# Kernel tuning notes

Hardware: AMD Instinct MI355X
Metric: run time of the kernel (lower is better)

## Reference

```python
import jax, jax.numpy as jnp
import numpy as np

B, SQ, SK, D, H = 4, 2048, 2048, 1024, 16
HD = D // H


def setup_inputs() -> dict:
    key = jax.random.key(0)
    ks = jax.random.split(key, 12)
    s = 1.0 / np.sqrt(D)
    return {
        "query": jax.random.normal(ks[0], (B, SQ, D), jnp.float32),
        "key": jax.random.normal(ks[1], (B, SK, D), jnp.float32),
        "value": jax.random.normal(ks[2], (B, SK, D), jnp.float32),
        "key_padding_mask": jax.random.randint(ks[3], (B, SK), 0, 2, jnp.int32),
        "Wq": jax.random.uniform(ks[4], (D, D), jnp.float32, -s, s),
        "bq": jnp.zeros((D,), jnp.float32),
        "Wk": jax.random.uniform(ks[5], (D, D), jnp.float32, -s, s),
        "bk": jnp.zeros((D,), jnp.float32),
        "Wv": jax.random.uniform(ks[6], (D, D), jnp.float32, -s, s),
        "bv": jnp.zeros((D,), jnp.float32),
        "Wo": jax.random.uniform(ks[7], (D, D), jnp.float32, -s, s),
        "bo": jnp.zeros((D,), jnp.float32),
    }


def reference(query, key, value, key_padding_mask, Wq, bq, Wk, bk, Wv, bv, Wo, bo):
    scale = HD ** -0.5
    # projections: torch Linear is x @ W.T + b
    q = (query @ Wq.T + bq).reshape(B, SQ, H, HD).transpose(0, 2, 1, 3)  # [B,H,SQ,HD]
    k = (key @ Wk.T + bk).reshape(B, SK, H, HD).transpose(0, 2, 1, 3)    # [B,H,SK,HD]
    v = (value @ Wv.T + bv).reshape(B, SK, H, HD).transpose(0, 2, 1, 3)  # [B,H,SK,HD]
    scores = jnp.einsum("bhqd,bhkd->bhqk", q, k) * scale                  # [B,H,SQ,SK]
    mask = key_padding_mask[:, None, None, :] != 0                        # True = keep
    scores = jnp.where(mask, scores, -jnp.inf)
    attn = jax.nn.softmax(scores, axis=-1)
    # dropout is identity at inference (eval mode)
    out = jnp.einsum("bhqk,bhkd->bhqd", attn, v)                          # [B,H,SQ,HD]
    out = out.transpose(0, 2, 1, 3).reshape(B, SQ, D)
    return out @ Wo.T + bo
```

## Files before the change

kernel.cpp:

```cpp
#include <hip/hip_runtime.h>


typedef __bf16 bf16_t;
typedef __attribute__((ext_vector_type(4))) __bf16 bf16x4;
typedef __attribute__((ext_vector_type(8))) __bf16 bf16x8;
typedef __attribute__((ext_vector_type(4))) float f32x4;

#define MFMA16(a, b, c) __builtin_amdgcn_mfma_f32_16x16x32_bf16(a, b, c, 0, 0, 0)

__device__ __forceinline__ void gl_lds16(const void* g, void* l) {
  __builtin_amdgcn_global_load_lds(
      (const __attribute__((address_space(1))) unsigned int*)g,
      (__attribute__((address_space(3))) unsigned int*)l, 16, 0, 0);
}

__global__ void wconv_kernel(const float* __restrict__ Wq, const float* __restrict__ Wk,
                             const float* __restrict__ Wv, const float* __restrict__ Wo,
                             bf16_t* __restrict__ out) {
  const int m = blockIdx.y;
  const float* src = (m == 0) ? Wq : (m == 1) ? Wk : (m == 2) ? Wv : Wo;
  bf16_t* dst = out + (size_t)m * (1024 * 1024);
  const int idx = (blockIdx.x * 256 + threadIdx.x) * 4;
  float4 v = *(const float4*)(src + idx);
  bf16x4 pk;
  pk[0] = (bf16_t)v.x; pk[1] = (bf16_t)v.y; pk[2] = (bf16_t)v.z; pk[3] = (bf16_t)v.w;
  *(bf16x4*)(dst + idx) = pk;
}

template <bool A_F32>
__global__ __launch_bounds__(256, 2) void gemm_kernel(
    const void* __restrict__ Aptr, const bf16_t* __restrict__ Bw,
    const float* __restrict__ bias, void* __restrict__ outp, const int out_mode) {
  __shared__ __align__(16) bf16_t As[2][16 * 512];
  __shared__ __align__(16) bf16_t Bs[2][16 * 512];

  const int tid = threadIdx.x;
  const int lane = tid & 63, wave = tid >> 6;
  const int fm = lane & 15, quad = lane >> 4;
  const int wr = wave >> 1, wc = wave & 1;
  const int m0 = blockIdx.x * 128, n0 = blockIdx.y * 128;

  f32x4 acc[4][4];
#pragma unroll
  for (int i = 0; i < 4; ++i)
#pragma unroll
    for (int j = 0; j < 4; ++j) acc[i][j] = f32x4{0.f, 0.f, 0.f, 0.f};

  auto stage = [&](int ks, int buf) {
    const int k0 = ks * 64;
    if constexpr (A_F32) {
      const float* A = (const float*)Aptr;
#pragma unroll
      for (int it = 0; it < 4; ++it) {
        const int fid = wave * 4 + it;
        const int row = (fid >> 1) * 16 + fm;
        const int col = (fid & 1) * 32 + quad * 8;
        const float* src = A + (size_t)(m0 + row) * 1024 + k0 + col;
        float4 v0 = *(const float4*)src, v1 = *(const float4*)(src + 4);
        bf16x8 pk;
        pk[0] = (bf16_t)v0.x; pk[1] = (bf16_t)v0.y; pk[2] = (bf16_t)v0.z; pk[3] = (bf16_t)v0.w;
        pk[4] = (bf16_t)v1.x; pk[5] = (bf16_t)v1.y; pk[6] = (bf16_t)v1.z; pk[7] = (bf16_t)v1.w;
        *(bf16x8*)(As[buf] + fid * 512 + lane * 8) = pk;
      }
    } else {
      const bf16_t* A = (const bf16_t*)Aptr;
#pragma unroll
      for (int it = 0; it < 4; ++it) {
        const int fid = wave * 4 + it;
        const int row = (fid >> 1) * 16 + fm;
        const int col = (fid & 1) * 32 + quad * 8;
        gl_lds16(A + (size_t)(m0 + row) * 1024 + k0 + col, As[buf] + fid * 512);
      }
    }
#pragma unroll
    for (int it = 0; it < 4; ++it) {
      const int fid = wave * 4 + it;
      const int row = (fid >> 1) * 16 + fm;
      const int col = (fid & 1) * 32 + quad * 8;
      gl_lds16(Bw + (size_t)(n0 + row) * 1024 + k0 + col, Bs[buf] + fid * 512);
    }
  };

  stage(0, 0);
  for (int ks = 0; ks < 16; ++ks) {
    __syncthreads();
    if (ks + 1 < 16) stage(ks + 1, (ks + 1) & 1);
    const bf16_t* Ab = As[ks & 1];
    const bf16_t* Bb = Bs[ks & 1];
#pragma unroll
    for (int u = 0; u < 2; ++u) {
      bf16x8 af[4], bfr[4];
#pragma unroll
      for (int i = 0; i < 4; ++i)
        af[i] = *(const bf16x8*)(Ab + ((4 * wr + i) * 2 + u) * 512 + lane * 8);
#pragma unroll
      for (int j = 0; j < 4; ++j)
        bfr[j] = *(const bf16x8*)(Bb + ((4 * wc + j) * 2 + u) * 512 + lane * 8);
#pragma unroll
      for (int i = 0; i < 4; ++i)
#pragma unroll
        for (int j = 0; j < 4; ++j) acc[i][j] = MFMA16(af[i], bfr[j], acc[i][j]);
    }
  }

  float bval[4];
#pragma unroll
  for (int j = 0; j < 4; ++j) bval[j] = bias[n0 + wc * 64 + j * 16 + fm];

#pragma unroll
  for (int i = 0; i < 4; ++i) {
#pragma unroll
    for (int j = 0; j < 4; ++j) {
      const int col = n0 + wc * 64 + j * 16 + fm;
#pragma unroll
      for (int r = 0; r < 4; ++r) {
        const int row = m0 + wr * 64 + i * 16 + quad * 4 + r;
        const float v = acc[i][j][r] + bval[j];
        if (out_mode == 2) {
          ((float*)outp)[(size_t)row * 1024 + col] = v;
        } else if (out_mode == 0) {
          ((bf16_t*)outp)[(size_t)row * 1024 + col] = (bf16_t)v;
        } else {
          const int bb = row >> 11, sk = row & 2047;
          const int tt = sk >> 7, L128 = sk & 127;
          const int c = L128 >> 5, hf = (L128 >> 4) & 1;
          const int qd = (L128 >> 2) & 3, rr = L128 & 3;
          const int hh = col >> 6, hd = col & 63;
          const int nt = hd >> 4, fv = hd & 15;
          const size_t idx = (((size_t)(bb * 16 + hh)) << 17) + tt * 8192 +
                             (nt * 4 + c) * 512 + (qd * 16 + fv) * 8 + hf * 4 + rr;
          ((bf16_t*)outp)[idx] = (bf16_t)v;
        }
      }
    }
  }
}

__global__ __launch_bounds__(256, 2) void attn_kernel(
    const bf16_t* __restrict__ q16, const bf16_t* __restrict__ k16,
    const bf16_t* __restrict__ vt16, const int* __restrict__ mask,
    bf16_t* __restrict__ o16) {
  __shared__ __align__(16) bf16_t Kb[2][8192];
  __shared__ __align__(16) bf16_t Vb[2][8192];
  __shared__ float mbuf[2][128];
  __shared__ float lbuf[128];

  const int tid = threadIdx.x;
  const int lane = tid & 63, wave = tid >> 6;
  const int fm = lane & 15, quad = lane >> 4;
  const int qt = blockIdx.x, bh = blockIdx.y;
  const int b = bh >> 4, h = bh & 15;
  const float SC = 0.125f * 1.44269504f;

  bf16x8 aq[2][2];
#pragma unroll
  for (int i = 0; i < 2; ++i)
#pragma unroll
    for (int dc = 0; dc < 2; ++dc) {
      const int row = qt * 128 + (2 * wave + i) * 16 + fm;
      aq[i][dc] = *(const bf16x8*)(q16 + ((size_t)(b * 2048 + row)) * 1024 + h * 64 +
                                   dc * 32 + quad * 8);
    }

  auto stageKV = [&](int t, int buf) {
    const bf16_t* kb = k16 + ((size_t)(b * 2048 + t * 128)) * 1024 + h * 64;
#pragma unroll
    for (int s = 0; s < 4; ++s) {
      const int fid = wave * 4 + s;
      const int row = (fid >> 1) * 16 + fm;
      const int col = (fid & 1) * 32 + quad * 8;
      gl_lds16(kb + (size_t)row * 1024 + col, Kb[buf] + fid * 512);
    }
    const bf16_t* vbase = vt16 + ((size_t)bh << 17) + t * 8192;
#pragma unroll
    for (int s = 0; s < 4; ++s) {
      const int fid = wave * 4 + s;
      gl_lds16(vbase + fid * 512 + lane * 8, Vb[buf] + fid * 512);
    }
    if (tid < 128) mbuf[buf][tid] = mask[b * 2048 + t * 128 + tid] ? 0.0f : -1e30f;
  };

  f32x4 oacc[2][4];
#pragma unroll
  for (int i = 0; i < 2; ++i)
#pragma unroll
    for (int n = 0; n < 4; ++n) oacc[i][n] = f32x4{0.f, 0.f, 0.f, 0.f};
  float lrow[2] = {0.f, 0.f};

  stageKV(0, 0);
  for (int t = 0; t < 16; ++t) {
    __syncthreads();
    if (t + 1 < 16) stageKV(t + 1, (t + 1) & 1);
    const bf16_t* K = Kb[t & 1];
    const bf16_t* V = Vb[t & 1];
    const float* mb = mbuf[t & 1];

    f32x4 sacc[2][8];
#pragma unroll
    for (int i = 0; i < 2; ++i)
#pragma unroll
      for (int j = 0; j < 8; ++j) sacc[i][j] = f32x4{0.f, 0.f, 0.f, 0.f};
#pragma unroll
    for (int j = 0; j < 8; ++j) {
#pragma unroll
      for (int dc = 0; dc < 2; ++dc) {
        bf16x8 kf = *(const bf16x8*)(K + (j * 2 + dc) * 512 + lane * 8);
        sacc[0][j] = MFMA16(kf, aq[0][dc], sacc[0][j]);
        sacc[1][j] = MFMA16(kf, aq[1][dc], sacc[1][j]);
      }
    }

#pragma unroll
    for (int j = 0; j < 8; ++j) {
      f32x4 md = *(const f32x4*)&mb[j * 16 + quad * 4];
#pragma unroll
      for (int i = 0; i < 2; ++i) {
#pragma unroll
        for (int r = 0; r < 4; ++r) {
          const float p = __builtin_amdgcn_exp2f(fmaf(sacc[i][j][r], SC, md[r]));
          sacc[i][j][r] = p;
          lrow[i] += p;
        }
      }
    }

#pragma unroll
    for (int c = 0; c < 4; ++c) {
      bf16x8 pf[2];
#pragma unroll
      for (int i = 0; i < 2; ++i) {
#pragma unroll
        for (int r = 0; r < 4; ++r) {
          pf[i][r] = (bf16_t)sacc[i][2 * c][r];
          pf[i][4 + r] = (bf16_t)sacc[i][2 * c + 1][r];
        }
      }
#pragma unroll
      for (int n = 0; n < 4; ++n) {
        bf16x8 vv = *(const bf16x8*)(V + (n * 4 + c) * 512 + lane * 8);
        oacc[0][n] = MFMA16(pf[0], vv, oacc[0][n]);
        oacc[1][n] = MFMA16(pf[1], vv, oacc[1][n]);
      }
    }
  }

#pragma unroll
  for (int i = 0; i < 2; ++i) {
    float l = lrow[i];
    l += __shfl_xor(l, 16);
    l += __shfl_xor(l, 32);
    if (quad == 0) lbuf[wave * 32 + i * 16 + fm] = l;
  }
  __syncthreads();
#pragma unroll
  for (int i = 0; i < 2; ++i) {
    f32x4 lv = *(const f32x4*)&lbuf[wave * 32 + i * 16 + quad * 4];
#pragma unroll
    for (int r = 0; r < 4; ++r) {
      const float inv = 1.0f / lv[r];
      const int row = qt * 128 + wave * 32 + i * 16 + quad * 4 + r;
#pragma unroll
      for (int n = 0; n < 4; ++n) {
        o16[((size_t)(b * 2048 + row)) * 1024 + h * 64 + n * 16 + fm] =
            (bf16_t)(oacc[i][n][r] * inv);
      }
    }
  }
}

extern "C" void kernel_launch(void* const* d_in, const int* in_sizes, int n_in,
                              void* d_out, int out_size, void* d_ws, size_t ws_size,
                              hipStream_t stream) {
  const float* query = (const float*)d_in[0];
  const float* key   = (const float*)d_in[1];
  const float* value = (const float*)d_in[2];
  const int* mask    = (const int*)d_in[3];
  const float* Wq = (const float*)d_in[4];
  const float* bq = (const float*)d_in[5];
  const float* Wk = (const float*)d_in[6];
  const float* bk = (const float*)d_in[7];
  const float* Wv = (const float*)d_in[8];
  const float* bv = (const float*)d_in[9];
  const float* Wo = (const float*)d_in[10];
  const float* bo = (const float*)d_in[11];

  char* ws = (char*)d_ws;
  bf16_t* W16  = (bf16_t*)ws;
  bf16_t* q16  = (bf16_t*)(ws + (size_t)8 * 1024 * 1024);
  bf16_t* k16  = q16 + 8388608;
  bf16_t* vt16 = k16 + 8388608;
  bf16_t* o16  = vt16 + 8388608;

  wconv_kernel<<<dim3(1024, 4), 256, 0, stream>>>(Wq, Wk, Wv, Wo, W16);
  gemm_kernel<true><<<dim3(64, 8), 256, 0, stream>>>(query, W16,           bq, q16,  0);
  gemm_kernel<true><<<dim3(64, 8), 256, 0, stream>>>(key,   W16 + 1048576, bk, k16,  0);
  gemm_kernel<true><<<dim3(64, 8), 256, 0, stream>>>(value, W16 + 2097152, bv, vt16, 1);
  attn_kernel<<<dim3(16, 64), 256, 0, stream>>>(q16, k16, vt16, mask, o16);
  gemm_kernel<false><<<dim3(64, 8), 256, 0, stream>>>(o16, W16 + 3145728, bo, d_out, 2);
}
```

Before: 420.3 us.

## Merge QKV projections, pipeline A loads via registers, restructure attention staging

Merges the three input projection GEMMs into a single launch with a z-dimension. The fp32 A tile is now loaded into registers before the MFMA loop and converted and written to LDS after it, so its global latency overlaps compute; packed bf16 conversion is used. In attention, V becomes single-buffered with an extra barrier to cut LDS and target three blocks per CU, the mask is loaded vectorized, and row sums come from an MFMA against ones instead of a shuffle reduction. The extra per-tile barrier and a single V buffer may expose more load latency.

```diff
diff --git a/kernel.cpp b/kernel.cpp
--- a/kernel.cpp
+++ b/kernel.cpp
@@ -2,6 +2,7 @@
 
 
 typedef __bf16 bf16_t;
+typedef __attribute__((ext_vector_type(2))) __bf16 bf16x2;
 typedef __attribute__((ext_vector_type(4))) __bf16 bf16x4;
 typedef __attribute__((ext_vector_type(8))) __bf16 bf16x8;
 typedef __attribute__((ext_vector_type(4))) float f32x4;
@@ -12,6 +13,17 @@
   __builtin_amdgcn_global_load_lds(
       (const __attribute__((address_space(1))) unsigned int*)g,
       (__attribute__((address_space(3))) unsigned int*)l, 16, 0, 0);
+}
+
+__device__ __forceinline__ bf16x2 cvt_pk_bf16(float a, float b) {
+#if __has_builtin(__builtin_amdgcn_cvt_pk_bf16_f32)
+  return __builtin_amdgcn_cvt_pk_bf16_f32(a, b);
+#else
+  bf16x2 r;
+  r[0] = (bf16_t)a;
+  r[1] = (bf16_t)b;
+  return r;
+#endif
 }
 
 __global__ void wconv_kernel(const float* __restrict__ Wq, const float* __restrict__ Wk,
@@ -27,12 +39,18 @@
   *(bf16x4*)(dst + idx) = pk;
 }
 
-template <bool A_F32>
-__global__ __launch_bounds__(256, 2) void gemm_kernel(
-    const void* __restrict__ Aptr, const bf16_t* __restrict__ Bw,
-    const float* __restrict__ bias, void* __restrict__ outp, const int out_mode) {
-  __shared__ __align__(16) bf16_t As[2][16 * 512];
-  __shared__ __align__(16) bf16_t Bs[2][16 * 512];
+__global__ __launch_bounds__(256, 2) void proj_kernel(
+    const float* __restrict__ Aq, const float* __restrict__ Ak, const float* __restrict__ Av,
+    const bf16_t* __restrict__ W16,
+    const float* __restrict__ bq, const float* __restrict__ bk, const float* __restrict__ bv,
+    bf16_t* __restrict__ q16, bf16_t* __restrict__ k16, bf16_t* __restrict__ vt16) {
+  __shared__ __align__(16) bf16_t As[2][8192];
+  __shared__ __align__(16) bf16_t Bs[2][8192];
+
+  const int z = blockIdx.z;
+  const float* A = (z == 0) ? Aq : (z == 1) ? Ak : Av;
+  const bf16_t* Bw = W16 + (size_t)z * 1048576;
+  const float* bias = (z == 0) ? bq : (z == 1) ? bk : bv;
 
   const int tid = threadIdx.x;
   const int lane = tid & 63, wave = tid >> 6;
@@ -46,45 +64,51 @@
 #pragma unroll
     for (int j = 0; j < 4; ++j) acc[i][j] = f32x4{0.f, 0.f, 0.f, 0.f};
 
-  auto stage = [&](int ks, int buf) {
-    const int k0 = ks * 64;
-    if constexpr (A_F32) {
-      const float* A = (const float*)Aptr;
-#pragma unroll
-      for (int it = 0; it < 4; ++it) {
-        const int fid = wave * 4 + it;
-        const int row = (fid >> 1) * 16 + fm;
-        const int col = (fid & 1) * 32 + quad * 8;
-        const float* src = A + (size_t)(m0 + row) * 1024 + k0 + col;
-        float4 v0 = *(const float4*)src, v1 = *(const float4*)(src + 4);
-        bf16x8 pk;
-        pk[0] = (bf16_t)v0.x; pk[1] = (bf16_t)v0.y; pk[2] = (bf16_t)v0.z; pk[3] = (bf16_t)v0.w;
-        pk[4] = (bf16_t)v1.x; pk[5] = (bf16_t)v1.y; pk[6] = (bf16_t)v1.z; pk[7] = (bf16_t)v1.w;
-        *(bf16x8*)(As[buf] + fid * 512 + lane * 8) = pk;
-      }
-    } else {
-      const bf16_t* A = (const bf16_t*)Aptr;
-#pragma unroll
-      for (int it = 0; it < 4; ++it) {
-        const int fid = wave * 4 + it;
-        const int row = (fid >> 1) * 16 + fm;
-        const int col = (fid & 1) * 32 + quad * 8;
-        gl_lds16(A + (size_t)(m0 + row) * 1024 + k0 + col, As[buf] + fid * 512);
-      }
-    }
+  float4 areg[4][2];
+  auto loadA = [&](int ks) {
 #pragma unroll
     for (int it = 0; it < 4; ++it) {
       const int fid = wave * 4 + it;
       const int row = (fid >> 1) * 16 + fm;
       const int col = (fid & 1) * 32 + quad * 8;
-      gl_lds16(Bw + (size_t)(n0 + row) * 1024 + k0 + col, Bs[buf] + fid * 512);
-    }
-  };
-
-  stage(0, 0);
+      const float* s = A + (size_t)(m0 + row) * 1024 + ks * 64 + col;
+      areg[it][0] = *(const float4*)s;
+      areg[it][1] = *(const float4*)(s + 4);
+    }
+  };
+  auto writeA = [&](int buf) {
+#pragma unroll
+    for (int it = 0; it < 4; ++it) {
+      const int fid = wave * 4 + it;
+      bf16x8 pk;
+      bf16x2* p2 = (bf16x2*)&pk;
+      p2[0] = cvt_pk_bf16(areg[it][0].x, areg[it][0].y);
+      p2[1] = cvt_pk_bf16(areg[it][0].z, areg[it][0].w);
+      p2[2] = cvt_pk_bf16(areg[it][1].x, areg[it][1].y);
+      p2[3] = cvt_pk_bf16(areg[it][1].z, areg[it][1].w);
+      *(bf16x8*)(As[buf] + fid * 512 + lane * 8) = pk;
+    }
+  };
+  auto dmaB = [&](int ks, int buf) {
+#pragma unroll
+    for (int it = 0; it < 4; ++it) {
+      const int fid = wave * 4 + it;
+      const int row = (fid >> 1) * 16 + fm;
+      const int col = (fid & 1) * 32 + quad * 8;
+      gl_lds16(Bw + (size_t)(n0 + row) * 1024 + ks * 64 + col, Bs[buf] + fid * 512);
+    }
+  };
+
+  loadA(0);
+  writeA(0);
+  dmaB(0, 0);
+
   for (int ks = 0; ks < 16; ++ks) {
     __syncthreads();
-    if (ks + 1 < 16) stage(ks + 1, (ks + 1) & 1);
+    if (ks < 15) {
+      loadA(ks + 1);
+      dmaB(ks + 1, (ks + 1) & 1);
+    }
     const bf16_t* Ab = As[ks & 1];
     const bf16_t* Bb = Bs[ks & 1];
 #pragma unroll
@@ -101,12 +125,14 @@
 #pragma unroll
         for (int j = 0; j < 4; ++j) acc[i][j] = MFMA16(af[i], bfr[j], acc[i][j]);
     }
+    if (ks < 15) writeA((ks + 1) & 1);
   }
 
   float bval[4];
 #pragma unroll
   for (int j = 0; j < 4; ++j) bval[j] = bias[n0 + wc * 64 + j * 16 + fm];
 
+  bf16_t* outp = (z == 0) ? q16 : (z == 1) ? k16 : vt16;
 #pragma unroll
   for (int i = 0; i < 4; ++i) {
 #pragma unroll
@@ -116,10 +142,8 @@
       for (int r = 0; r < 4; ++r) {
         const int row = m0 + wr * 64 + i * 16 + quad * 4 + r;
         const float v = acc[i][j][r] + bval[j];
-        if (out_mode == 2) {
-          ((float*)outp)[(size_t)row * 1024 + col] = v;
-        } else if (out_mode == 0) {
-          ((bf16_t*)outp)[(size_t)row * 1024 + col] = (bf16_t)v;
+        if (z != 2) {
+          outp[(size_t)row * 1024 + col] = (bf16_t)v;
         } else {
           const int bb = row >> 11, sk = row & 2047;
           const int tt = sk >> 7, L128 = sk & 127;
@@ -129,21 +153,87 @@
           const int nt = hd >> 4, fv = hd & 15;
           const size_t idx = (((size_t)(bb * 16 + hh)) << 17) + tt * 8192 +
                              (nt * 4 + c) * 512 + (qd * 16 + fv) * 8 + hf * 4 + rr;
-          ((bf16_t*)outp)[idx] = (bf16_t)v;
+          outp[idx] = (bf16_t)v;
         }
       }
     }
   }
 }
 
-__global__ __launch_bounds__(256, 2) void attn_kernel(
+__global__ __launch_bounds__(256, 2) void oproj_kernel(
+    const bf16_t* __restrict__ A, const bf16_t* __restrict__ Bw,
+    const float* __restrict__ bias, float* __restrict__ outp) {
+  __shared__ __align__(16) bf16_t As[2][8192];
+  __shared__ __align__(16) bf16_t Bs[2][8192];
+
+  const int tid = threadIdx.x;
+  const int lane = tid & 63, wave = tid >> 6;
+  const int fm = lane & 15, quad = lane >> 4;
+  const int wr = wave >> 1, wc = wave & 1;
+  const int m0 = blockIdx.x * 128, n0 = blockIdx.y * 128;
+
+  f32x4 acc[4][4];
+#pragma unroll
+  for (int i = 0; i < 4; ++i)
+#pragma unroll
+    for (int j = 0; j < 4; ++j) acc[i][j] = f32x4{0.f, 0.f, 0.f, 0.f};
+
+  auto stage = [&](int ks, int buf) {
+#pragma unroll
+    for (int it = 0; it < 4; ++it) {
+      const int fid = wave * 4 + it;
+      const int row = (fid >> 1) * 16 + fm;
+      const int col = (fid & 1) * 32 + quad * 8;
+      gl_lds16(A + (size_t)(m0 + row) * 1024 + ks * 64 + col, As[buf] + fid * 512);
+      gl_lds16(Bw + (size_t)(n0 + row) * 1024 + ks * 64 + col, Bs[buf] + fid * 512);
+    }
+  };
+
+  stage(0, 0);
+  for (int ks = 0; ks < 16; ++ks) {
+    __syncthreads();
+    if (ks < 15) stage(ks + 1, (ks + 1) & 1);
+    const bf16_t* Ab = As[ks & 1];
+    const bf16_t* Bb = Bs[ks & 1];
+#pragma unroll
+    for (int u = 0; u < 2; ++u) {
+      bf16x8 af[4], bfr[4];
+#pragma unroll
+      for (int i = 0; i < 4; ++i)
+        af[i] = *(const bf16x8*)(Ab + ((4 * wr + i) * 2 + u) * 512 + lane * 8);
+#pragma unroll
+      for (int j = 0; j < 4; ++j)
+        bfr[j] = *(const bf16x8*)(Bb + ((4 * wc + j) * 2 + u) * 512 + lane * 8);
+#pragma unroll
+      for (int i = 0; i < 4; ++i)
+#pragma unroll
+        for (int j = 0; j < 4; ++j) acc[i][j] = MFMA16(af[i], bfr[j], acc[i][j]);
+    }
+  }
+
+  float bval[4];
+#pragma unroll
+  for (int j = 0; j < 4; ++j) bval[j] = bias[n0 + wc * 64 + j * 16 + fm];
+#pragma unroll
+  for (int i = 0; i < 4; ++i)
+#pragma unroll
+    for (int j = 0; j < 4; ++j) {
+      const int col = n0 + wc * 64 + j * 16 + fm;
+#pragma unroll
+      for (int r = 0; r < 4; ++r) {
+        const int row = m0 + wr * 64 + i * 16 + quad * 4 + r;
+        outp[(size_t)row * 1024 + col] = acc[i][j][r] + bval[j];
+      }
+    }
+}
+
+__global__ __launch_bounds__(256, 3) void attn_kernel(
     const bf16_t* __restrict__ q16, const bf16_t* __restrict__ k16,
     const bf16_t* __restrict__ vt16, const int* __restrict__ mask,
     bf16_t* __restrict__ o16) {
   __shared__ __align__(16) bf16_t Kb[2][8192];
-  __shared__ __align__(16) bf16_t Vb[2][8192];
-  __shared__ float mbuf[2][128];
-  __shared__ float lbuf[128];
+  __shared__ __align__(16) bf16_t Vb[8192];
+  __shared__ float mb[2][128];
 
   const int tid = threadIdx.x;
   const int lane = tid & 63, wave = tid >> 6;
@@ -162,7 +252,7 @@
                                    dc * 32 + quad * 8);
     }
 
-  auto stageKV = [&](int t, int buf) {
+  auto dmaK = [&](int t, int buf) {
     const bf16_t* kb = k16 + ((size_t)(b * 2048 + t * 128)) * 1024 + h * 64;
 #pragma unroll
     for (int s = 0; s < 4; ++s) {
@@ -171,13 +261,22 @@
       const int col = (fid & 1) * 32 + quad * 8;
       gl_lds16(kb + (size_t)row * 1024 + col, Kb[buf] + fid * 512);
     }
-    const bf16_t* vbase = vt16 + ((size_t)bh << 17) + t * 8192;
+  };
+  auto dmaV = [&](int t) {
+    const bf16_t* vb = vt16 + ((size_t)bh << 17) + t * 8192;
 #pragma unroll
     for (int s = 0; s < 4; ++s) {
       const int fid = wave * 4 + s;
-      gl_lds16(vbase + fid * 512 + lane * 8, Vb[buf] + fid * 512);
-    }
-    if (tid < 128) mbuf[buf][tid] = mask[b * 2048 + t * 128 + tid] ? 0.0f : -1e30f;
+      gl_lds16(vb + fid * 512 + lane * 8, Vb + fid * 512);
+    }
+  };
+  auto stageM = [&](int t) {
+    if (tid < 32) {
+      int4 m4 = *(const int4*)(mask + b * 2048 + t * 128 + tid * 4);
+      float4 f{m4.x ? 0.f : -1e30f, m4.y ? 0.f : -1e30f, m4.z ? 0.f : -1e30f,
+               m4.w ? 0.f : -1e30f};
+      *(float4*)&mb[t & 1][tid * 4] = f;
+    }
   };
 
   f32x4 oacc[2][4];
@@ -185,15 +284,18 @@
   for (int i = 0; i < 2; ++i)
 #pragma unroll
     for (int n = 0; n < 4; ++n) oacc[i][n] = f32x4{0.f, 0.f, 0.f, 0.f};
-  float lrow[2] = {0.f, 0.f};
-
-  stageKV(0, 0);
+  f32x4 lacc[2] = {f32x4{0.f, 0.f, 0.f, 0.f}, f32x4{0.f, 0.f, 0.f, 0.f}};
+  bf16x8 ones;
+#pragma unroll
+  for (int e = 0; e < 8; ++e) ones[e] = (bf16_t)1.0f;
+
+  dmaK(0, 0);
+  stageM(0);
+
   for (int t = 0; t < 16; ++t) {
     __syncthreads();
-    if (t + 1 < 16) stageKV(t + 1, (t + 1) & 1);
+    dmaV(t);
     const bf16_t* K = Kb[t & 1];
-    const bf16_t* V = Vb[t & 1];
-    const float* mb = mbuf[t & 1];
 
     f32x4 sacc[2][8];
 #pragma unroll
@@ -210,18 +312,20 @@
       }
     }
 
+    const float* mrow = mb[t & 1];
 #pragma unroll
     for (int j = 0; j < 8; ++j) {
-      f32x4 md = *(const f32x4*)&mb[j * 16 + quad * 4];
-#pragma unroll
-      for (int i = 0; i < 2; ++i) {
-#pragma unroll
-        for (int r = 0; r < 4; ++r) {
-          const float p = __builtin_amdgcn_exp2f(fmaf(sacc[i][j][r], SC, md[r]));
-          sacc[i][j][r] = p;
-          lrow[i] += p;
-        }
-      }
+      f32x4 md = *(const f32x4*)&mrow[j * 16 + quad * 4];
+#pragma unroll
+      for (int i = 0; i < 2; ++i)
+#pragma unroll
+        for (int r = 0; r < 4; ++r)
+          sacc[i][j][r] = __builtin_amdgcn_exp2f(fmaf(sacc[i][j][r], SC, md[r]));
+    }
+    __syncthreads();
+    if (t < 15) {
+      dmaK(t + 1, (t + 1) & 1);
+      stageM(t + 1);
     }
 
 #pragma unroll
@@ -229,35 +333,28 @@
       bf16x8 pf[2];
 #pragma unroll
       for (int i = 0; i < 2; ++i) {
-#pragma unroll
-        for (int r = 0; r < 4; ++r) {
-          pf[i][r] = (bf16_t)sacc[i][2 * c][r];
-          pf[i][4 + r] = (bf16_t)sacc[i][2 * c + 1][r];
-        }
+        bf16x2* p2 = (bf16x2*)&pf[i];
+        p2[0] = cvt_pk_bf16(sacc[i][2 * c][0], sacc[i][2 * c][1]);
+        p2[1] = cvt_pk_bf16(sacc[i][2 * c][2], sacc[i][2 * c][3]);
+        p2[2] = cvt_pk_bf16(sacc[i][2 * c + 1][0], sacc[i][2 * c + 1][1]);
+        p2[3] = cvt_pk_bf16(sacc[i][2 * c + 1][2], sacc[i][2 * c + 1][3]);
       }
 #pragma unroll
       for (int n = 0; n < 4; ++n) {
-        bf16x8 vv = *(const bf16x8*)(V + (n * 4 + c) * 512 + lane * 8);
+        bf16x8 vv = *(const bf16x8*)(Vb + (n * 4 + c) * 512 + lane * 8);
         oacc[0][n] = MFMA16(pf[0], vv, oacc[0][n]);
         oacc[1][n] = MFMA16(pf[1], vv, oacc[1][n]);
       }
+      lacc[0] = MFMA16(pf[0], ones, lacc[0]);
+      lacc[1] = MFMA16(pf[1], ones, lacc[1]);
     }
   }
 
 #pragma unroll
   for (int i = 0; i < 2; ++i) {
-    float l = lrow[i];
-    l += __shfl_xor(l, 16);
-    l += __shfl_xor(l, 32);
-    if (quad == 0) lbuf[wave * 32 + i * 16 + fm] = l;
-  }
-  __syncthreads();
-#pragma unroll
-  for (int i = 0; i < 2; ++i) {
-    f32x4 lv = *(const f32x4*)&lbuf[wave * 32 + i * 16 + quad * 4];
 #pragma unroll
     for (int r = 0; r < 4; ++r) {
-      const float inv = 1.0f / lv[r];
+      const float inv = 1.0f / lacc[i][r];
       const int row = qt * 128 + wave * 32 + i * 16 + quad * 4 + r;
 #pragma unroll
       for (int n = 0; n < 4; ++n) {
@@ -292,9 +389,8 @@
   bf16_t* o16  = vt16 + 8388608;
 
   wconv_kernel<<<dim3(1024, 4), 256, 0, stream>>>(Wq, Wk, Wv, Wo, W16);
-  gemm_kernel<true><<<dim3(64, 8), 256, 0, stream>>>(query, W16,           bq, q16,  0);
-  gemm_kernel<true><<<dim3(64, 8), 256, 0, stream>>>(key,   W16 + 1048576, bk, k16,  0);
-  gemm_kernel<true><<<dim3(64, 8), 256, 0, stream>>>(value, W16 + 2097152, bv, vt16, 1);
+  proj_kernel<<<dim3(64, 8, 3), 256, 0, stream>>>(query, key, value, W16, bq, bk, bv,
+                                                  q16, k16, vt16);
   attn_kernel<<<dim3(16, 64), 256, 0, stream>>>(q16, k16, vt16, mask, o16);
-  gemm_kernel<false><<<dim3(64, 8), 256, 0, stream>>>(o16, W16 + 3145728, bo, d_out, 2);
-}
+  oproj_kernel<<<dim3(64, 8), 256, 0, stream>>>(o16, W16 + 3145728, bo, (float*)d_out);
+}
```

After: 465.2 us. 10.7% more time.
